# Optimization experiments

Measured on AMD Instinct MI355X. Metric: run time of the kernel, lower is better.

Reference implementation:

```python
import jax, jax.numpy as jnp
import numpy as np

T, N, C, J = 128, 16, 1, 8192
V_TH = 1.0  # IFNode default threshold; v_reset = 0.0 (hard reset)


def setup_inputs() -> dict:
    key = jax.random.key(0)
    k1, = jax.random.split(key, 1)
    inp = jax.random.uniform(k1, (T, N, C, J), dtype=jnp.float32)
    lateral_weight = jnp.full((J,), 10.0, dtype=jnp.float32)
    return {"input": inp, "lateral_weight": lateral_weight}


def _spike(x):
    # Heaviside forward (ATan surrogate only matters for backward).
    return (x >= 0.0).astype(x.dtype)


def reference(input, lateral_weight):
    # input: (T, N, C, J); lateral_weight: (J,)
    w = lateral_weight

    def step(carry, x_t):
        h, y_prev, v = carry
        # h = h - (1 - y_prev) * h + w * y_prev  ==  y_prev * (h + w)
        h = y_prev * h + w * y_prev
        x = x_t + h
        v = v + x                      # IF integration
        s = _spike(v - V_TH)           # spike = (v >= v_th)
        v = v * (1.0 - s)              # hard reset to v_reset = 0
        return (h, s, v), s

    z = jnp.zeros(input.shape[1:], dtype=input.dtype)  # (N, C, J)
    (_, _, _), y_seq = jax.lax.scan(step, (z, z, z), input)
    return y_seq  # (T, N, C, J) == y_seq[1:] in the torch code
```

## Files before the change

### kernel.cpp

```cpp
#include <hip/hip_runtime.h>


#define T_STEPS 128
#define J_DIM   8192
#define NCJ     131072
#define NCJ4    (NCJ / 4)
#define U       8

typedef float v4f __attribute__((ext_vector_type(4)));

__global__ __launch_bounds__(64) void SpikeAmplifier_73452530696745_kernel(
    const float* __restrict__ in,
    const float* __restrict__ w,
    float* __restrict__ out)
{
    const int idx4 = blockIdx.x * blockDim.x + threadIdx.x;
    const int jbase = (idx4 * 4) & (J_DIM - 1);
    const v4f wv = *(const v4f*)&w[jbase];

    const v4f* __restrict__ in4  = (const v4f*)in;
    v4f* __restrict__       out4 = (v4f*)out;

    v4f h = {0.f, 0.f, 0.f, 0.f};
    v4f y = {0.f, 0.f, 0.f, 0.f};
    v4f v = {0.f, 0.f, 0.f, 0.f};

    v4f xbuf[U];
    int off = idx4;
    #pragma unroll
    for (int u = 0; u < U; ++u)
        xbuf[u] = __builtin_nontemporal_load(&in4[off + u * NCJ4]);

    constexpr int NBLK = T_STEPS / U;
    for (int blk = 0; blk < NBLK; ++blk) {
        v4f xnext[U];
        const int nextbase = off + U * NCJ4;
        if (blk + 1 < NBLK) {
            #pragma unroll
            for (int u = 0; u < U; ++u)
                xnext[u] = __builtin_nontemporal_load(&in4[nextbase + u * NCJ4]);
        }

        #pragma unroll
        for (int u = 0; u < U; ++u) {
            v4f yv;
            #pragma unroll
            for (int e = 0; e < 4; ++e) {
                h[e] = y[e] * h[e] + wv[e] * y[e];
                const float x = xbuf[u][e] + h[e];
                v[e] = v[e] + x;
                const bool s = (v[e] >= 1.0f);
                y[e] = s ? 1.0f : 0.0f;
                v[e] = s ? 0.0f : v[e];
                yv[e] = y[e];
            }
            __builtin_nontemporal_store(yv, &out4[off + u * NCJ4]);
        }

        off = nextbase;
        #pragma unroll
        for (int u = 0; u < U; ++u) xbuf[u] = xnext[u];
    }
}

extern "C" void kernel_launch(void* const* d_in, const int* in_sizes, int n_in,
                              void* d_out, int out_size, void* d_ws, size_t ws_size,
                              hipStream_t stream) {
    const float* in  = (const float*)d_in[0];
    const float* w   = (const float*)d_in[1];
    float*       out = (float*)d_out;

    SpikeAmplifier_73452530696745_kernel<<<NCJ4 / 64, 64, 0, stream>>>(in, w, out);
}
```

Measured before the change: 118.1 us.

## Use float2 per thread with deeper rolling prefetch and peeled final block

Each thread now handles 2 neurons (float2) instead of 4, which doubles the thread count to 1024 blocks for more parallelism and memory-level concurrency. The prefetch depth grows to 16 timesteps and moves into a rolling per-timestep scheme that replaces the next-block buffer, and the last block is peeled so no branch guards the loads. Accesses become 8-byte rather than 16-byte, which may lower per-instruction efficiency.

```diff
diff --git a/kernel.cpp b/kernel.cpp
--- a/kernel.cpp
+++ b/kernel.cpp
@@ -4,62 +4,81 @@
 #define T_STEPS 128
 #define J_DIM   8192
 #define NCJ     131072
-#define NCJ4    (NCJ / 4)
-#define U       8
+#define NCJ2    (NCJ / 2)
+#define U       16
 
-typedef float v4f __attribute__((ext_vector_type(4)));
+typedef float v2f __attribute__((ext_vector_type(2)));
 
 __global__ __launch_bounds__(64) void SpikeAmplifier_73452530696745_kernel(
     const float* __restrict__ in,
     const float* __restrict__ w,
     float* __restrict__ out)
 {
-    const int idx4 = blockIdx.x * blockDim.x + threadIdx.x;
-    const int jbase = (idx4 * 4) & (J_DIM - 1);
-    const v4f wv = *(const v4f*)&w[jbase];
+    const int idx2 = blockIdx.x * blockDim.x + threadIdx.x;
+    const int jbase = (idx2 * 2) & (J_DIM - 1);
+    const v2f wv = *(const v2f*)&w[jbase];
 
-    const v4f* __restrict__ in4  = (const v4f*)in;
-    v4f* __restrict__       out4 = (v4f*)out;
+    const v2f* __restrict__ in2  = (const v2f*)in;
+    v2f* __restrict__       out2 = (v2f*)out;
 
-    v4f h = {0.f, 0.f, 0.f, 0.f};
-    v4f y = {0.f, 0.f, 0.f, 0.f};
-    v4f v = {0.f, 0.f, 0.f, 0.f};
+    v2f h = {0.f, 0.f};
+    v2f y = {0.f, 0.f};
+    v2f v = {0.f, 0.f};
 
-    v4f xbuf[U];
-    int off = idx4;
-    #pragma unroll
-    for (int u = 0; u < U; ++u)
-        xbuf[u] = __builtin_nontemporal_load(&in4[off + u * NCJ4]);
+    v2f xbuf[U];
+    {
+        const v2f* p = in2 + idx2;
+        #pragma unroll
+        for (int u = 0; u < U; ++u) {
+            xbuf[u] = __builtin_nontemporal_load(p);
+            p += NCJ2;
+        }
+    }
+
+    const v2f* pld = in2 + idx2 + (size_t)U * NCJ2;
+    v2f*       pst = out2 + idx2;
 
     constexpr int NBLK = T_STEPS / U;
-    for (int blk = 0; blk < NBLK; ++blk) {
-        v4f xnext[U];
-        const int nextbase = off + U * NCJ4;
-        if (blk + 1 < NBLK) {
-            #pragma unroll
-            for (int u = 0; u < U; ++u)
-                xnext[u] = __builtin_nontemporal_load(&in4[nextbase + u * NCJ4]);
-        }
 
+    for (int blk = 0; blk < NBLK - 1; ++blk) {
         #pragma unroll
         for (int u = 0; u < U; ++u) {
-            v4f yv;
+            const v2f xt = xbuf[u];
+            xbuf[u] = __builtin_nontemporal_load(pld);
+            pld += NCJ2;
+
+            v2f yv;
             #pragma unroll
-            for (int e = 0; e < 4; ++e) {
+            for (int e = 0; e < 2; ++e) {
                 h[e] = y[e] * h[e] + wv[e] * y[e];
-                const float x = xbuf[u][e] + h[e];
+                const float x = xt[e] + h[e];
                 v[e] = v[e] + x;
                 const bool s = (v[e] >= 1.0f);
                 y[e] = s ? 1.0f : 0.0f;
                 v[e] = s ? 0.0f : v[e];
                 yv[e] = y[e];
             }
-            __builtin_nontemporal_store(yv, &out4[off + u * NCJ4]);
+            __builtin_nontemporal_store(yv, pst);
+            pst += NCJ2;
         }
+    }
 
-        off = nextbase;
+    #pragma unroll
+    for (int u = 0; u < U; ++u) {
+        const v2f xt = xbuf[u];
+        v2f yv;
         #pragma unroll
-        for (int u = 0; u < U; ++u) xbuf[u] = xnext[u];
+        for (int e = 0; e < 2; ++e) {
+            h[e] = y[e] * h[e] + wv[e] * y[e];
+            const float x = xt[e] + h[e];
+            v[e] = v[e] + x;
+            const bool s = (v[e] >= 1.0f);
+            y[e] = s ? 1.0f : 0.0f;
+            v[e] = s ? 0.0f : v[e];
+            yv[e] = y[e];
+        }
+        __builtin_nontemporal_store(yv, pst);
+        pst += NCJ2;
     }
 }
 
@@ -70,5 +89,5 @@
     const float* w   = (const float*)d_in[1];
     float*       out = (float*)d_out;
 
-    SpikeAmplifier_73452530696745_kernel<<<NCJ4 / 64, 64, 0, stream>>>(in, w, out);
+    SpikeAmplifier_73452530696745_kernel<<<NCJ2 / 64, 64, 0, stream>>>(in, w, out);
 }
```

Result: no change. 118.6 us (+0.4%).
